# Kernel tuning notes

Measured on AMD Instinct MI355X. Metric: run time of the kernel, lower is better.

## Reference

```python
import jax, jax.numpy as jnp
import numpy as np

B_BOXES = 2          # boxes per cell (b in source)
NUM_CLASSES = 20     # pred channels = B_BOXES*5 + NUM_CLASSES = 30
LAMBDA_COORD = 5.0
LAMBDA_NOOBJ = 0.5


def setup_inputs() -> dict:
    key = jax.random.key(0)
    k1, k2, k3 = jax.random.split(key, 3)
    N, S = 16384, 7
    preds = jax.random.uniform(k1, (N, S, S, B_BOXES * 5 + NUM_CLASSES), dtype=jnp.float32)
    targets = jax.random.uniform(k2, (N, S, S, 5 + NUM_CLASSES), dtype=jnp.float32)
    # channel 0 of target is the object indicator c (checked via c == 1)
    obj = (jax.random.uniform(k3, (N, S, S)) < 0.3).astype(jnp.float32)
    targets = targets.at[..., 0].set(obj)
    return {"preds": preds, "targets": targets}


def reference(preds, targets):
    # preds: [N,S,S,30]; targets: [N,S,S,25]
    N, S1, S2, _ = preds.shape
    bboxes = preds[..., : B_BOXES * 5].reshape(N, S1, S2, B_BOXES, 5)
    obj_scores = bboxes[..., 0]                         # [N,S,S,B]
    idx = jnp.argmax(obj_scores, axis=-1)               # [N,S,S] best box by confidence
    best = jnp.take_along_axis(bboxes, idx[..., None, None], axis=3)[..., 0, :]  # [N,S,S,5]

    c_mask = (targets[..., 0] == 1.0)                   # object present per cell

    box_loss = jnp.sum((best[..., 1:5] - targets[..., 1:5]) ** 2, axis=-1)
    pc_loss = (best[..., 0] - targets[..., 0]) ** 2
    class_loss = jnp.sum((preds[..., B_BOXES * 5:] - targets[..., 5:]) ** 2, axis=-1)

    obj_term = LAMBDA_COORD * box_loss + pc_loss + class_loss
    noobj_term = LAMBDA_NOOBJ * jnp.sum(obj_scores ** 2, axis=-1)

    loss = jnp.sum(jnp.where(c_mask, obj_term, noobj_term))
    return loss
```

## Files before the change

kernel.cpp:

```cpp
#include <hip/hip_runtime.h>

#define LAMBDA_COORD 5.0f
#define LAMBDA_NOOBJ 0.5f


typedef float f4u __attribute__((ext_vector_type(4), aligned(4)));
typedef float f2u __attribute__((ext_vector_type(2), aligned(4)));

__global__ void zero_out_kernel(float* out, int n) {
    int i = blockIdx.x * blockDim.x + threadIdx.x;
    if (i < n) out[i] = 0.0f;
}

__global__ __launch_bounds__(256, 6) void yolo_loss_kernel(
    const float* __restrict__ preds, const float* __restrict__ targets,
    float* __restrict__ out, int n_cells)
{
    __shared__ float s_part[4];
    const int tid = threadIdx.x;
    const int c = blockIdx.x * 256 + tid;

    float loss = 0.0f;
    if (c < n_cells) {
        const float* pbase = preds + (size_t)c * 30;
        const float* tbase = targets + (size_t)c * 25;
        const f4u* pp = (const f4u*)pbase;
        const f4u* tp = (const f4u*)tbase;

        f4u P0 = pp[0], P1 = pp[1], P2 = pp[2], P3 = pp[3];
        f4u P4 = pp[4], P5 = pp[5], P6 = pp[6];
        f2u P7 = *(const f2u*)(pbase + 28);
        f4u T0 = tp[0], T1 = tp[1], T2 = tp[2], T3 = tp[3];
        f4u T4 = tp[4], T5 = tp[5];
        float t24 = tbase[24];

        float p0 = P0.x, p5c = P1.y;
        bool pick1 = p5c > p0;
        float b0 = pick1 ? p5c  : p0;
        float b1 = pick1 ? P1.z : P0.y;
        float b2 = pick1 ? P1.w : P0.z;
        float b3 = pick1 ? P2.x : P0.w;
        float b4 = pick1 ? P2.y : P1.x;

        float t0 = T0.x;
        float d1 = b1 - T0.y, d2 = b2 - T0.z, d3 = b3 - T0.w, d4 = b4 - T1.x;
        float box_loss = d1 * d1 + d2 * d2 + d3 * d3 + d4 * d4;
        float dpc = b0 - t0;
        float pc_loss = dpc * dpc;

        float cl = 0.0f, d;
        d = P2.z - T1.y; cl += d * d;
        d = P2.w - T1.z; cl += d * d;
        d = P3.x - T1.w; cl += d * d;
        d = P3.y - T2.x; cl += d * d;
        d = P3.z - T2.y; cl += d * d;
        d = P3.w - T2.z; cl += d * d;
        d = P4.x - T2.w; cl += d * d;
        d = P4.y - T3.x; cl += d * d;
        d = P4.z - T3.y; cl += d * d;
        d = P4.w - T3.z; cl += d * d;
        d = P5.x - T3.w; cl += d * d;
        d = P5.y - T4.x; cl += d * d;
        d = P5.z - T4.y; cl += d * d;
        d = P5.w - T4.z; cl += d * d;
        d = P6.x - T4.w; cl += d * d;
        d = P6.y - T5.x; cl += d * d;
        d = P6.z - T5.y; cl += d * d;
        d = P6.w - T5.z; cl += d * d;
        d = P7.x - T5.w; cl += d * d;
        d = P7.y - t24;  cl += d * d;

        float obj_term = LAMBDA_COORD * box_loss + pc_loss + cl;
        float noobj_term = LAMBDA_NOOBJ * (p0 * p0 + p5c * p5c);
        loss = (t0 == 1.0f) ? obj_term : noobj_term;
    }

    #pragma unroll
    for (int off = 32; off > 0; off >>= 1)
        loss += __shfl_down(loss, off, 64);

    const int wave = tid >> 6;
    if ((tid & 63) == 0) s_part[wave] = loss;
    __syncthreads();
    if (tid == 0) {
        float s = s_part[0] + s_part[1] + s_part[2] + s_part[3];
        atomicAdd(out, s);
    }
}

extern "C" void kernel_launch(void* const* d_in, const int* in_sizes, int n_in,
                              void* d_out, int out_size, void* d_ws, size_t ws_size,
                              hipStream_t stream) {
    const float* preds   = (const float*)d_in[0];
    const float* targets = (const float*)d_in[1];
    float* out = (float*)d_out;

    const int n_cells = in_sizes[0] / 30;

    zero_out_kernel<<<(out_size + 255) / 256, 256, 0, stream>>>(out, out_size);

    const int grid = (n_cells + 255) / 256;
    yolo_loss_kernel<<<grid, 256, 0, stream>>>(preds, targets, out, n_cells);
}
```

Before: 194.0 us.

## Stage block inputs into LDS with coalesced global_load_lds before per-cell compute

For full blocks, each block copies its contiguous preds and targets slab into shared memory using 16-byte direct global-to-LDS loads. These loads are fully coalesced, unlike the earlier per-thread strided vector loads that were only 4-byte aligned. Each thread then reads its cell's fields from LDS. This uses about 56 KB of LDS per block and lowers occupancy (launch bounds 256,2), and the strided LDS reads may cause bank conflicts. Partial tail blocks keep the old direct-load path.

```diff
diff --git a/kernel.cpp b/kernel.cpp
--- a/kernel.cpp
+++ b/kernel.cpp
@@ -12,67 +12,127 @@
     if (i < n) out[i] = 0.0f;
 }
 
-__global__ __launch_bounds__(256, 6) void yolo_loss_kernel(
+__device__ __forceinline__ void gld16(const float* g, float* l) {
+    __builtin_amdgcn_global_load_lds(
+        (const __attribute__((address_space(1))) void*)g,
+        (__attribute__((address_space(3))) void*)l,
+        16, 0, 0);
+}
+
+__global__ __launch_bounds__(256, 2) void yolo_loss_kernel(
     const float* __restrict__ preds, const float* __restrict__ targets,
     float* __restrict__ out, int n_cells)
 {
+    __shared__ float sp[256 * 30];
+    __shared__ float st[256 * 25];
     __shared__ float s_part[4];
+
     const int tid = threadIdx.x;
-    const int c = blockIdx.x * 256 + tid;
+    const int block0 = blockIdx.x * 256;
+    const bool full = (block0 + 256) <= n_cells;
 
     float loss = 0.0f;
-    if (c < n_cells) {
-        const float* pbase = preds + (size_t)c * 30;
-        const float* tbase = targets + (size_t)c * 25;
-        const f4u* pp = (const f4u*)pbase;
-        const f4u* tp = (const f4u*)tbase;
 
-        f4u P0 = pp[0], P1 = pp[1], P2 = pp[2], P3 = pp[3];
-        f4u P4 = pp[4], P5 = pp[5], P6 = pp[6];
-        f2u P7 = *(const f2u*)(pbase + 28);
-        f4u T0 = tp[0], T1 = tp[1], T2 = tp[2], T3 = tp[3];
-        f4u T4 = tp[4], T5 = tp[5];
-        float t24 = tbase[24];
+    if (full) {
+        const float* pblk = preds + (size_t)block0 * 30;
+        const float* tblk = targets + (size_t)block0 * 25;
 
-        float p0 = P0.x, p5c = P1.y;
-        bool pick1 = p5c > p0;
-        float b0 = pick1 ? p5c  : p0;
-        float b1 = pick1 ? P1.z : P0.y;
-        float b2 = pick1 ? P1.w : P0.z;
-        float b3 = pick1 ? P2.x : P0.w;
-        float b4 = pick1 ? P2.y : P1.x;
+        #pragma unroll
+        for (int j = 0; j < 8; ++j) {
+            int i = tid + j * 256;
+            if (i < 1920) gld16(pblk + i * 4, sp + i * 4);
+        }
+        #pragma unroll
+        for (int j = 0; j < 7; ++j) {
+            int i = tid + j * 256;
+            if (i < 1600) gld16(tblk + i * 4, st + i * 4);
+        }
+        __syncthreads();
 
-        float t0 = T0.x;
-        float d1 = b1 - T0.y, d2 = b2 - T0.z, d3 = b3 - T0.w, d4 = b4 - T1.x;
+        const float* P = sp + tid * 30;
+        const float* T = st + tid * 25;
+
+        float q0 = P[0], q1 = P[1], q2 = P[2], q3 = P[3], q4 = P[4];
+        float q5 = P[5], q6 = P[6], q7 = P[7], q8 = P[8], q9 = P[9];
+
+        bool pick1 = q5 > q0;
+        float b0 = pick1 ? q5 : q0;
+        float b1 = pick1 ? q6 : q1;
+        float b2 = pick1 ? q7 : q2;
+        float b3 = pick1 ? q8 : q3;
+        float b4 = pick1 ? q9 : q4;
+
+        float t0 = T[0];
+        float d1 = b1 - T[1], d2 = b2 - T[2], d3 = b3 - T[3], d4 = b4 - T[4];
         float box_loss = d1 * d1 + d2 * d2 + d3 * d3 + d4 * d4;
         float dpc = b0 - t0;
         float pc_loss = dpc * dpc;
 
-        float cl = 0.0f, d;
-        d = P2.z - T1.y; cl += d * d;
-        d = P2.w - T1.z; cl += d * d;
-        d = P3.x - T1.w; cl += d * d;
-        d = P3.y - T2.x; cl += d * d;
-        d = P3.z - T2.y; cl += d * d;
-        d = P3.w - T2.z; cl += d * d;
-        d = P4.x - T2.w; cl += d * d;
-        d = P4.y - T3.x; cl += d * d;
-        d = P4.z - T3.y; cl += d * d;
-        d = P4.w - T3.z; cl += d * d;
-        d = P5.x - T3.w; cl += d * d;
-        d = P5.y - T4.x; cl += d * d;
-        d = P5.z - T4.y; cl += d * d;
-        d = P5.w - T4.z; cl += d * d;
-        d = P6.x - T4.w; cl += d * d;
-        d = P6.y - T5.x; cl += d * d;
-        d = P6.z - T5.y; cl += d * d;
-        d = P6.w - T5.z; cl += d * d;
-        d = P7.x - T5.w; cl += d * d;
-        d = P7.y - t24;  cl += d * d;
+        float cl = 0.0f;
+        #pragma unroll
+        for (int k = 0; k < 20; ++k) {
+            float d = P[10 + k] - T[5 + k];
+            cl += d * d;
+        }
 
         float obj_term = LAMBDA_COORD * box_loss + pc_loss + cl;
-        float noobj_term = LAMBDA_NOOBJ * (p0 * p0 + p5c * p5c);
+        float noobj_term = LAMBDA_NOOBJ * (q0 * q0 + q5 * q5);
         loss = (t0 == 1.0f) ? obj_term : noobj_term;
+    } else {
+        const int c = block0 + tid;
+        if (c < n_cells) {
+            const float* pbase = preds + (size_t)c * 30;
+            const float* tbase = targets + (size_t)c * 25;
+            const f4u* pp = (const f4u*)pbase;
+            const f4u* tp = (const f4u*)tbase;
+
+            f4u P0 = pp[0], P1 = pp[1], P2 = pp[2], P3 = pp[3];
+            f4u P4 = pp[4], P5 = pp[5], P6 = pp[6];
+            f2u P7 = *(const f2u*)(pbase + 28);
+            f4u T0 = tp[0], T1 = tp[1], T2 = tp[2], T3 = tp[3];
+            f4u T4 = tp[4], T5 = tp[5];
+            float t24 = tbase[24];
+
+            float p0 = P0.x, p5c = P1.y;
+            bool pick1 = p5c > p0;
+            float b0 = pick1 ? p5c  : p0;
+            float b1 = pick1 ? P1.z : P0.y;
+            float b2 = pick1 ? P1.w : P0.z;
+            float b3 = pick1 ? P2.x : P0.w;
+            float b4 = pick1 ? P2.y : P1.x;
+
+            float t0 = T0.x;
+            float d1 = b1 - T0.y, d2 = b2 - T0.z, d3 = b3 - T0.w, d4 = b4 - T1.x;
+            float box_loss = d1 * d1 + d2 * d2 + d3 * d3 + d4 * d4;
+            float dpc = b0 - t0;
+            float pc_loss = dpc * dpc;
+
+            float cl = 0.0f, d;
+            d = P2.z - T1.y; cl += d * d;
+            d = P2.w - T1.z; cl += d * d;
+            d = P3.x - T1.w; cl += d * d;
+            d = P3.y - T2.x; cl += d * d;
+            d = P3.z - T2.y; cl += d * d;
+            d = P3.w - T2.z; cl += d * d;
+            d = P4.x - T2.w; cl += d * d;
+            d = P4.y - T3.x; cl += d * d;
+            d = P4.z - T3.y; cl += d * d;
+            d = P4.w - T3.z; cl += d * d;
+            d = P5.x - T3.w; cl += d * d;
+            d = P5.y - T4.x; cl += d * d;
+            d = P5.z - T4.y; cl += d * d;
+            d = P5.w - T4.z; cl += d * d;
+            d = P6.x - T4.w; cl += d * d;
+            d = P6.y - T5.x; cl += d * d;
+            d = P6.z - T5.y; cl += d * d;
+            d = P6.w - T5.z; cl += d * d;
+            d = P7.x - T5.w; cl += d * d;
+            d = P7.y - t24;  cl += d * d;
+
+            float obj_term = LAMBDA_COORD * box_loss + pc_loss + cl;
+            float noobj_term = LAMBDA_NOOBJ * (p0 * p0 + p5c * p5c);
+            loss = (t0 == 1.0f) ? obj_term : noobj_term;
+        }
     }
 
     #pragma unroll
```

Measured after the change: 194.8 us. No clear change (+0.4%).

## Stage preds/targets through LDS with coalesced float4 loads per block

Applied to the files above, without the earlier changes.

Each full block now loads its contiguous 256-cell slab of preds and targets with fully coalesced float4 loads into shared memory, then each thread reads its own cell from LDS. This replaces per-thread strided, misaligned vector loads (stride of 30 and 25 floats), which waste cache-line bandwidth and issue more transactions. The cost is about 56KB of LDS per block, a barrier, and launch bounds lowered to 2 blocks per CU, which may limit latency hiding. Partial tail blocks keep the old direct path.

```diff
diff --git a/kernel.cpp b/kernel.cpp
--- a/kernel.cpp
+++ b/kernel.cpp
@@ -4,6 +4,7 @@
 #define LAMBDA_NOOBJ 0.5f
 
 
+typedef float f4 __attribute__((ext_vector_type(4)));
 typedef float f4u __attribute__((ext_vector_type(4), aligned(4)));
 typedef float f2u __attribute__((ext_vector_type(2), aligned(4)));
 
@@ -12,67 +13,143 @@
     if (i < n) out[i] = 0.0f;
 }
 
-__global__ __launch_bounds__(256, 6) void yolo_loss_kernel(
+__global__ __launch_bounds__(256, 2) void yolo_loss_kernel(
     const float* __restrict__ preds, const float* __restrict__ targets,
     float* __restrict__ out, int n_cells)
 {
+    __shared__ f4 sp4[1920];
+    __shared__ f4 st4[1600];
     __shared__ float s_part[4];
+
     const int tid = threadIdx.x;
-    const int c = blockIdx.x * 256 + tid;
+    const int block0 = blockIdx.x * 256;
+    const bool full = (block0 + 256) <= n_cells;
 
     float loss = 0.0f;
-    if (c < n_cells) {
-        const float* pbase = preds + (size_t)c * 30;
-        const float* tbase = targets + (size_t)c * 25;
-        const f4u* pp = (const f4u*)pbase;
-        const f4u* tp = (const f4u*)tbase;
 
-        f4u P0 = pp[0], P1 = pp[1], P2 = pp[2], P3 = pp[3];
-        f4u P4 = pp[4], P5 = pp[5], P6 = pp[6];
-        f2u P7 = *(const f2u*)(pbase + 28);
-        f4u T0 = tp[0], T1 = tp[1], T2 = tp[2], T3 = tp[3];
-        f4u T4 = tp[4], T5 = tp[5];
-        float t24 = tbase[24];
+    if (full) {
+        const f4* pg = (const f4*)(preds + (size_t)block0 * 30);
+        const f4* tg = (const f4*)(targets + (size_t)block0 * 25);
 
-        float p0 = P0.x, p5c = P1.y;
-        bool pick1 = p5c > p0;
-        float b0 = pick1 ? p5c  : p0;
-        float b1 = pick1 ? P1.z : P0.y;
-        float b2 = pick1 ? P1.w : P0.z;
-        float b3 = pick1 ? P2.x : P0.w;
-        float b4 = pick1 ? P2.y : P1.x;
+        f4 a0 = pg[tid];
+        f4 a1 = pg[tid + 256];
+        f4 a2 = pg[tid + 512];
+        f4 a3 = pg[tid + 768];
+        f4 a4 = pg[tid + 1024];
+        f4 a5 = pg[tid + 1280];
+        f4 a6 = pg[tid + 1536];
+        f4 a7;
+        if (tid < 128) a7 = pg[tid + 1792];
+        f4 b0 = tg[tid];
+        f4 b1 = tg[tid + 256];
+        f4 b2 = tg[tid + 512];
+        f4 b3 = tg[tid + 768];
+        f4 b4 = tg[tid + 1024];
+        f4 b5 = tg[tid + 1280];
+        f4 b6;
+        if (tid < 64) b6 = tg[tid + 1536];
 
-        float t0 = T0.x;
-        float d1 = b1 - T0.y, d2 = b2 - T0.z, d3 = b3 - T0.w, d4 = b4 - T1.x;
+        sp4[tid]        = a0;
+        sp4[tid + 256]  = a1;
+        sp4[tid + 512]  = a2;
+        sp4[tid + 768]  = a3;
+        sp4[tid + 1024] = a4;
+        sp4[tid + 1280] = a5;
+        sp4[tid + 1536] = a6;
+        if (tid < 128) sp4[tid + 1792] = a7;
+        st4[tid]        = b0;
+        st4[tid + 256]  = b1;
+        st4[tid + 512]  = b2;
+        st4[tid + 768]  = b3;
+        st4[tid + 1024] = b4;
+        st4[tid + 1280] = b5;
+        if (tid < 64) st4[tid + 1536] = b6;
+        __syncthreads();
+
+        const float* P = (const float*)sp4 + tid * 30;
+        const float* T = (const float*)st4 + tid * 25;
+
+        float q0 = P[0], q1 = P[1], q2 = P[2], q3 = P[3], q4 = P[4];
+        float q5 = P[5], q6 = P[6], q7 = P[7], q8 = P[8], q9 = P[9];
+
+        bool pick1 = q5 > q0;
+        float c0 = pick1 ? q5 : q0;
+        float c1 = pick1 ? q6 : q1;
+        float c2 = pick1 ? q7 : q2;
+        float c3 = pick1 ? q8 : q3;
+        float c4 = pick1 ? q9 : q4;
+
+        float t0 = T[0];
+        float d1 = c1 - T[1], d2 = c2 - T[2], d3 = c3 - T[3], d4 = c4 - T[4];
         float box_loss = d1 * d1 + d2 * d2 + d3 * d3 + d4 * d4;
-        float dpc = b0 - t0;
+        float dpc = c0 - t0;
         float pc_loss = dpc * dpc;
 
-        float cl = 0.0f, d;
-        d = P2.z - T1.y; cl += d * d;
-        d = P2.w - T1.z; cl += d * d;
-        d = P3.x - T1.w; cl += d * d;
-        d = P3.y - T2.x; cl += d * d;
-        d = P3.z - T2.y; cl += d * d;
-        d = P3.w - T2.z; cl += d * d;
-        d = P4.x - T2.w; cl += d * d;
-        d = P4.y - T3.x; cl += d * d;
-        d = P4.z - T3.y; cl += d * d;
-        d = P4.w - T3.z; cl += d * d;
-        d = P5.x - T3.w; cl += d * d;
-        d = P5.y - T4.x; cl += d * d;
-        d = P5.z - T4.y; cl += d * d;
-        d = P5.w - T4.z; cl += d * d;
-        d = P6.x - T4.w; cl += d * d;
-        d = P6.y - T5.x; cl += d * d;
-        d = P6.z - T5.y; cl += d * d;
-        d = P6.w - T5.z; cl += d * d;
-        d = P7.x - T5.w; cl += d * d;
-        d = P7.y - t24;  cl += d * d;
+        float cl = 0.0f;
+        #pragma unroll
+        for (int k = 0; k < 20; ++k) {
+            float d = P[10 + k] - T[5 + k];
+            cl += d * d;
+        }
 
         float obj_term = LAMBDA_COORD * box_loss + pc_loss + cl;
-        float noobj_term = LAMBDA_NOOBJ * (p0 * p0 + p5c * p5c);
+        float noobj_term = LAMBDA_NOOBJ * (q0 * q0 + q5 * q5);
         loss = (t0 == 1.0f) ? obj_term : noobj_term;
+    } else {
+        const int c = block0 + tid;
+        if (c < n_cells) {
+            const float* pbase = preds + (size_t)c * 30;
+            const float* tbase = targets + (size_t)c * 25;
+            const f4u* pp = (const f4u*)pbase;
+            const f4u* tp = (const f4u*)tbase;
+
+            f4u P0 = pp[0], P1 = pp[1], P2 = pp[2], P3 = pp[3];
+            f4u P4 = pp[4], P5 = pp[5], P6 = pp[6];
+            f2u P7 = *(const f2u*)(pbase + 28);
+            f4u T0 = tp[0], T1 = tp[1], T2 = tp[2], T3 = tp[3];
+            f4u T4 = tp[4], T5 = tp[5];
+            float t24 = tbase[24];
+
+            float p0 = P0.x, p5c = P1.y;
+            bool pick1 = p5c > p0;
+            float c0 = pick1 ? p5c  : p0;
+            float c1 = pick1 ? P1.z : P0.y;
+            float c2 = pick1 ? P1.w : P0.z;
+            float c3 = pick1 ? P2.x : P0.w;
+            float c4 = pick1 ? P2.y : P1.x;
+
+            float t0 = T0.x;
+            float d1 = c1 - T0.y, d2 = c2 - T0.z, d3 = c3 - T0.w, d4 = c4 - T1.x;
+            float box_loss = d1 * d1 + d2 * d2 + d3 * d3 + d4 * d4;
+            float dpc = c0 - t0;
+            float pc_loss = dpc * dpc;
+
+            float cl = 0.0f, d;
+            d = P2.z - T1.y; cl += d * d;
+            d = P2.w - T1.z; cl += d * d;
+            d = P3.x - T1.w; cl += d * d;
+            d = P3.y - T2.x; cl += d * d;
+            d = P3.z - T2.y; cl += d * d;
+            d = P3.w - T2.z; cl += d * d;
+            d = P4.x - T2.w; cl += d * d;
+            d = P4.y - T3.x; cl += d * d;
+            d = P4.z - T3.y; cl += d * d;
+            d = P4.w - T3.z; cl += d * d;
+            d = P5.x - T3.w; cl += d * d;
+            d = P5.y - T4.x; cl += d * d;
+            d = P5.z - T4.y; cl += d * d;
+            d = P5.w - T4.z; cl += d * d;
+            d = P6.x - T4.w; cl += d * d;
+            d = P6.y - T5.x; cl += d * d;
+            d = P6.z - T5.y; cl += d * d;
+            d = P6.w - T5.z; cl += d * d;
+            d = P7.x - T5.w; cl += d * d;
+            d = P7.y - t24;  cl += d * d;
+
+            float obj_term = LAMBDA_COORD * box_loss + pc_loss + cl;
+            float noobj_term = LAMBDA_NOOBJ * (p0 * p0 + p5c * p5c);
+            loss = (t0 == 1.0f) ? obj_term : noobj_term;
+        }
     }
 
     #pragma unroll
```

Result: no change. 195.9 us (+1.0%).
